# Kernel tuning notes

Measured on AMD Instinct MI355X. Metric: run time of the kernel, lower is better.

## Reference

```python
import jax, jax.numpy as jnp
import numpy as np

N = 200000
MESH = (128, 128, 128)   # mesh_dimensions
P = 4                    # spline_order
ALPHA = 0.35             # Ewald splitting parameter (1/Angstrom)
KE = 14.3996             # coulomb_constant, eV*A/e^2
BOX = 128.0              # cubic box edge, Angstrom


def _bspline(u, n):
    """Cardinal B-spline M_n(u), support [0, n]. Recursion depth = n-2 (static)."""
    if n == 2:
        return jnp.clip(1.0 - jnp.abs(u - 1.0), 0.0, 1.0)
    return (u * _bspline(u, n - 1) + (n - u) * _bspline(u - 1.0, n - 1)) / (n - 1)


def _spread_weights(frac_d, K):
    """Per-dimension P spline weights and wrapped grid indices for each atom."""
    u = frac_d * K
    base = jnp.floor(u)
    j = jnp.arange(P, dtype=frac_d.dtype)
    # evaluation points t_j = (u - base) + (P-1) - j, each in (0, P)
    t = (u - base)[:, None] + (P - 1) - j                      # [N, P]
    w = _bspline(t, P)                                         # [N, P]
    idx = (base.astype(jnp.int32)[:, None] - (P - 1)
           + jnp.arange(P, dtype=jnp.int32)) % K               # [N, P]
    return w, idx


def _bmod2(K):
    """|b(m)|^2 Euler exponential-spline factors for one mesh dimension."""
    m = (jnp.fft.fftfreq(K) * K).astype(jnp.float32)
    k = jnp.arange(P - 1, dtype=jnp.float32)
    Mv = _bspline(k + 1.0, P)                                  # M_P(1..P-1)
    D = (Mv[None, :] * jnp.exp(2j * jnp.pi * m[:, None] * k[None, :] / K)).sum(-1)
    return (1.0 / jnp.maximum(jnp.abs(D) ** 2, 1e-12)).astype(jnp.float32)


def _pme_energy(positions, charges, cell):
    Kx, Ky, Kz = MESH
    cellinv = jnp.linalg.inv(cell)
    V = jnp.abs(jnp.linalg.det(cell))
    frac = (positions @ cellinv) % 1.0                         # [N, 3]

    # --- B-spline charge spreading (scatter) ---
    wx, ix = _spread_weights(frac[:, 0], Kx)
    wy, iy = _spread_weights(frac[:, 1], Ky)
    wz, iz = _spread_weights(frac[:, 2], Kz)
    w3 = (charges[:, None, None, None]
          * wx[:, :, None, None] * wy[:, None, :, None] * wz[:, None, None, :])
    lin = (ix[:, :, None, None] * Ky + iy[:, None, :, None]) * Kz + iz[:, None, None, :]
    Q = (jnp.zeros(Kx * Ky * Kz, dtype=positions.dtype)
         .at[lin.reshape(-1)].add(w3.reshape(-1))
         .reshape(MESH))

    # --- reciprocal space ---
    S = jnp.fft.fftn(Q)
    S2 = (S * jnp.conj(S)).real                                # |F[Q]|^2
    b3 = (_bmod2(Kx)[:, None, None] * _bmod2(Ky)[None, :, None]
          * _bmod2(Kz)[None, None, :])
    mx = (jnp.fft.fftfreq(Kx) * Kx).astype(positions.dtype)
    my = (jnp.fft.fftfreq(Ky) * Ky).astype(positions.dtype)
    mz = (jnp.fft.fftfreq(Kz) * Kz).astype(positions.dtype)
    mg = jnp.stack(jnp.meshgrid(mx, my, mz, indexing='ij'), axis=-1)  # [Kx,Ky,Kz,3]
    kvec = 2.0 * jnp.pi * jnp.einsum('xyzm,nm->xyzn', mg, cellinv)
    k2 = (kvec ** 2).sum(-1)
    G = jnp.where(k2 > 0.0,
                  jnp.exp(-k2 / (4.0 * ALPHA ** 2)) / jnp.where(k2 > 0.0, k2, 1.0),
                  0.0)
    e_rec = KE * (2.0 * jnp.pi / V) * (G * b3 * S2).sum()
    e_self = -KE * ALPHA / jnp.sqrt(jnp.pi).astype(positions.dtype) * (charges ** 2).sum()
    return e_rec + e_self


def setup_inputs() -> dict:
    key = jax.random.key(0)
    k1, k2 = jax.random.split(key)
    positions = jax.random.uniform(k1, (N, 3), dtype=jnp.float32) * BOX
    charges = jax.random.normal(k2, (N,), dtype=jnp.float32) * 0.5
    charges = charges - charges.mean()   # neutral system (k=0 mode excluded)
    cell = jnp.eye(3, dtype=jnp.float32) * BOX
    return {"positions": positions, "charges": charges, "cell": cell}


def reference(positions, charges, cell):
    # energy [B=1, 1] and analytic forces [N, 3] via force gather (dE/dr)
    e, g = jax.value_and_grad(lambda p: _pme_energy(p, charges, cell))(positions)
    return (jnp.reshape(e, (1, 1)), -g)
```

## Files before the change

### kernel.cpp

```cpp
#include <hip/hip_runtime.h>

#define KDIM 128
#define NTOT (KDIM * KDIM * KDIM)
#define BPD 16
#define NBINS (BPD * BPD * BPD)
#define TILE_D 11
#define T2 (TILE_D * TILE_D)
#define TILE_N (TILE_D * TILE_D * TILE_D)
#define TPAD 1332
#define TSTRIDE 1344
#define CHUNK 256
#define NZKEEP 65
#define NSCALE_BLK (NZKEEP * 8)
#define ST 17
#define ZST 17

static constexpr float PI_F = 3.14159265358979323846f;
static constexpr float TWO_PI_F = 6.28318530717958647692f;
static constexpr float KE_F = 14.3996f;
static constexpr float ALPHA_F = 0.35f;

__device__ __forceinline__ int brev7(int i) { return (int)(__brev((unsigned)i) >> 25); }

struct pf4 { float a, b, c, d; };
__device__ __forceinline__ pf4 ld4u(const float* p) {
    pf4 v;
    __builtin_memcpy(&v, p, 16);
    return v;
}

__device__ __forceinline__ void inv3x3(const float* c, float* inv, float* adet) {
    float a00 = c[0], a01 = c[1], a02 = c[2];
    float a10 = c[3], a11 = c[4], a12 = c[5];
    float a20 = c[6], a21 = c[7], a22 = c[8];
    float det = a00 * (a11 * a22 - a12 * a21) - a01 * (a10 * a22 - a12 * a20) +
                a02 * (a10 * a21 - a11 * a20);
    float id = 1.0f / det;
    inv[0] = (a11 * a22 - a12 * a21) * id;
    inv[1] = (a02 * a21 - a01 * a22) * id;
    inv[2] = (a01 * a12 - a02 * a11) * id;
    inv[3] = (a12 * a20 - a10 * a22) * id;
    inv[4] = (a00 * a22 - a02 * a20) * id;
    inv[5] = (a02 * a10 - a00 * a12) * id;
    inv[6] = (a10 * a21 - a11 * a20) * id;
    inv[7] = (a01 * a20 - a00 * a21) * id;
    inv[8] = (a00 * a11 - a01 * a10) * id;
    *adet = fabsf(det);
}

__device__ __forceinline__ void bspline4(float f, float* w, float* dw) {
    float f2 = f * f, f3 = f2 * f;
    float omf = 1.0f - f;
    w[0] = omf * omf * omf * (1.0f / 6.0f);
    w[1] = (3.0f * f3 - 6.0f * f2 + 4.0f) * (1.0f / 6.0f);
    w[2] = (-3.0f * f3 + 3.0f * f2 + 3.0f * f + 1.0f) * (1.0f / 6.0f);
    w[3] = f3 * (1.0f / 6.0f);
    dw[0] = -0.5f * omf * omf;
    dw[1] = 1.5f * f2 - 2.0f * f;
    dw[2] = -1.5f * f2 + f + 0.5f;
    dw[3] = 0.5f * f2;
}

__device__ __forceinline__ void atom_base(const float* __restrict__ pos, const float* inv,
                                          int i, int base[3], float fpart[3]) {
    float p0 = pos[3 * i], p1 = pos[3 * i + 1], p2 = pos[3 * i + 2];
#pragma unroll
    for (int d = 0; d < 3; d++) {
        float fr = p0 * inv[d] + p1 * inv[3 + d] + p2 * inv[6 + d];
        fr -= floorf(fr);
        float u = fr * (float)KDIM;
        float bs = floorf(u);
        fpart[d] = u - bs;
        int b = (int)bs;
        base[d] = b & (KDIM - 1);
    }
}

__device__ __forceinline__ float bmod2f(int x) {
    float th = (TWO_PI_F / (float)KDIM) * (float)x;
    float s1, c1, s2, c2;
    __sincosf(th, &s1, &c1);
    __sincosf(th + th, &s2, &c2);
    float dr = 0.16666667f + 0.66666667f * c1 + 0.16666667f * c2;
    float di = 0.66666667f * s1 + 0.16666667f * s2;
    float d2 = dr * dr + di * di;
    return 1.0f / fmaxf(d2, 1e-12f);
}

__global__ __launch_bounds__(256) void zero_tbl_kernel(int* __restrict__ counts,
                                                       int* __restrict__ cursor,
                                                       float* __restrict__ mtblS,
                                                       float* __restrict__ btblS) {
    int i = blockIdx.x * 256 + threadIdx.x;
    if (i < NBINS) {
        counts[i] = 0;
        cursor[i] = 0;
    }
    if (blockIdx.x == 0 && threadIdx.x < KDIM) {
        int r = brev7(threadIdx.x);
        mtblS[threadIdx.x] = (float)(r < 64 ? r : r - 128);
        btblS[threadIdx.x] = bmod2f(r);
    }
}

__global__ __launch_bounds__(256) void hist_kernel(const float* __restrict__ pos,
                                                   const float* __restrict__ chg,
                                                   const float* __restrict__ cell,
                                                   int* __restrict__ counts,
                                                   float* __restrict__ q2_part, int n) {
    __shared__ float hred[4];
    int i = blockIdx.x * blockDim.x + threadIdx.x;
    float q2 = 0.0f;
    if (i < n) {
        float inv[9], det;
        inv3x3(cell, inv, &det);
        int base[3];
        float fp[3];
        atom_base(pos, inv, i, base, fp);
        int bid = ((base[0] >> 3) << 8) | ((base[1] >> 3) << 4) | (base[2] >> 3);
        atomicAdd(&counts[bid], 1);
        float qi = chg[i];
        q2 = qi * qi;
    }
#pragma unroll
    for (int off = 32; off; off >>= 1) q2 += __shfl_down(q2, off);
    if ((threadIdx.x & 63) == 0) hred[threadIdx.x >> 6] = q2;
    __syncthreads();
    if (threadIdx.x == 0) q2_part[blockIdx.x] = hred[0] + hred[1] + hred[2] + hred[3];
}

__global__ __launch_bounds__(256) void scan_kernel(const int* __restrict__ counts,
                                                   int* __restrict__ starts) {
    __shared__ int part[256];
    int tid = threadIdx.x;
    int local[NBINS / 256];
    int sum = 0;
#pragma unroll
    for (int k = 0; k < NBINS / 256; k++) {
        local[k] = counts[tid * (NBINS / 256) + k];
        sum += local[k];
    }
    part[tid] = sum;
    __syncthreads();
    if (tid == 0) {
        int acc = 0;
        for (int i = 0; i < 256; i++) {
            int t = part[i];
            part[i] = acc;
            acc += t;
        }
        starts[NBINS] = acc;
    }
    __syncthreads();
    int acc = part[tid];
#pragma unroll
    for (int k = 0; k < NBINS / 256; k++) {
        starts[tid * (NBINS / 256) + k] = acc;
        acc += local[k];
    }
}

__global__ __launch_bounds__(256) void scatter_kernel(const float* __restrict__ pos,
                                                      const float* __restrict__ chg,
                                                      const float* __restrict__ cell,
                                                      const int* __restrict__ starts,
                                                      int* __restrict__ cursor,
                                                      float* __restrict__ records,
                                                      int* __restrict__ binatoms, int n) {
    int i = blockIdx.x * blockDim.x + threadIdx.x;
    if (i >= n) return;
    float inv[9], det;
    inv3x3(cell, inv, &det);
    int base[3];
    float fp[3];
    atom_base(pos, inv, i, base, fp);
    int bid = ((base[0] >> 3) << 8) | ((base[1] >> 3) << 4) | (base[2] >> 3);
    int slot = atomicAdd(&cursor[bid], 1) + starts[bid];
    binatoms[slot] = i;
    int loc = (base[0] & 7) | ((base[1] & 7) << 4) | ((base[2] & 7) << 8);
    float4* rec = (float4*)(records + (size_t)slot * 8);
    rec[0] = make_float4(fp[0], fp[1], fp[2], chg[i]);
    rec[1] = make_float4(__int_as_float(loc), 0.0f, 0.0f, 0.0f);
}

__global__ __launch_bounds__(256) void spread_bins_kernel(
    const float* __restrict__ records, const int* __restrict__ starts,
    float* __restrict__ tiles) {
    __shared__ float tile4[4 * TPAD];
    __shared__ float4 arec[CHUNK * 4];
    int tid = threadIdx.x;
    int bid = blockIdx.x;
    for (int i = tid; i < 4 * TPAD; i += 256) tile4[i] = 0.0f;
    int s = starts[bid], e = starts[bid + 1];
    int w = tid >> 6, l = tid & 63;
    int j0 = l >> 4, j1 = (l >> 2) & 3, j2 = l & 3;
    int joff = j0 * T2 + j1 * TILE_D + j2;
    float* mytile = tile4 + w * TPAD;
    for (int c0 = s; c0 < e; c0 += CHUNK) {
        int cnt = min(CHUNK, e - c0);
        __syncthreads();
        if (tid < cnt) {
            const float4* rp = (const float4*)records + (size_t)(c0 + tid) * 2;
            float4 r0 = rp[0];
            float4 r1 = rp[1];
            float wv[4], dv[4];
            bspline4(r0.x, wv, dv);
            arec[tid * 4 + 0] =
                make_float4(r0.w * wv[0], r0.w * wv[1], r0.w * wv[2], r0.w * wv[3]);
            bspline4(r0.y, wv, dv);
            arec[tid * 4 + 1] = make_float4(wv[0], wv[1], wv[2], wv[3]);
            bspline4(r0.z, wv, dv);
            arec[tid * 4 + 2] = make_float4(wv[0], wv[1], wv[2], wv[3]);
            arec[tid * 4 + 3] = r1;
        }
        __syncthreads();
        for (int a = w; a < cnt; a += 4) {
            const float* A = (const float*)&arec[a << 2];
            float val = A[j0] * A[4 + j1] * A[8 + j2];
            int lc = __float_as_int(A[12]);
            int tb = (lc & 15) * T2 + ((lc >> 4) & 15) * TILE_D + ((lc >> 8) & 15);
            mytile[tb + joff] += val;
        }
    }
    __syncthreads();
    float* tout = tiles + (size_t)bid * TSTRIDE;
    for (int i = tid; i < TILE_N; i += 256)
        tout[i] = tile4[i] + tile4[TPAD + i] + tile4[2 * TPAD + i] + tile4[3 * TPAD + i];
}

__device__ __forceinline__ float2 cmul(float2 a, float cs, float sn) {
    return make_float2(a.x * cs - a.y * sn, a.x * sn + a.y * cs);
}

__device__ __forceinline__ void wave_fft128_dif(float2& v0, float2& v1, int l, float sign) {
    {
        float ang = sign * (PI_F / 64.0f) * (float)l;
        float sn, cs;
        __sincosf(ang, &sn, &cs);
        float2 d = make_float2(v0.x - v1.x, v0.y - v1.y);
        v0 = make_float2(v0.x + v1.x, v0.y + v1.y);
        v1 = cmul(d, cs, sn);
    }
#pragma unroll
    for (int m = 32; m >= 1; m >>= 1) {
        float ang = sign * (PI_F / (float)m) * (float)(l & (m - 1));
        float sn, cs;
        __sincosf(ang, &sn, &cs);
        bool hi = (l & m) != 0;
        float2 p0, p1;
        p0.x = __shfl_xor(v0.x, m);
        p0.y = __shfl_xor(v0.y, m);
        p1.x = __shfl_xor(v1.x, m);
        p1.y = __shfl_xor(v1.y, m);
        float2 a0 = hi ? cmul(make_float2(p0.x - v0.x, p0.y - v0.y), cs, sn)
                       : make_float2(v0.x + p0.x, v0.y + p0.y);
        float2 a1 = hi ? cmul(make_float2(p1.x - v1.x, p1.y - v1.y), cs, sn)
                       : make_float2(v1.x + p1.x, v1.y + p1.y);
        v0 = a0;
        v1 = a1;
    }
}

__device__ __forceinline__ void wave_fft128_dit(float2& v0, float2& v1, int l, float sign) {
#pragma unroll
    for (int m = 1; m <= 32; m <<= 1) {
        float2 p0, p1;
        p0.x = __shfl_xor(v0.x, m);
        p0.y = __shfl_xor(v0.y, m);
        p1.x = __shfl_xor(v1.x, m);
        p1.y = __shfl_xor(v1.y, m);
        float ang = sign * (PI_F / (float)m) * (float)(l & (m - 1));
        float sn, cs;
        __sincosf(ang, &sn, &cs);
        bool hi = (l & m) != 0;
        float2 o0 = hi ? v0 : p0, e0 = hi ? p0 : v0;
        float2 o1 = hi ? v1 : p1, e1 = hi ? p1 : v1;
        float2 t0 = cmul(o0, cs, sn);
        float2 t1 = cmul(o1, cs, sn);
        float s = hi ? -1.0f : 1.0f;
        v0 = make_float2(e0.x + s * t0.x, e0.y + s * t0.y);
        v1 = make_float2(e1.x + s * t1.x, e1.y + s * t1.y);
    }
    float ang = sign * (PI_F / 64.0f) * (float)l;
    float sn, cs;
    __sincosf(ang, &sn, &cs);
    float2 t = cmul(v1, cs, sn);
    float2 e = v0;
    v0 = make_float2(e.x + t.x, e.y + t.y);
    v1 = make_float2(e.x - t.x, e.y - t.y);
}

__device__ __forceinline__ float merge_val(const float* __restrict__ tiles, int nx, int ny,
                                           const int* bxs, const int* lxs, const int* bys,
                                           const int* lys, int gz) {
    int bz = gz >> 3, oz = gz & 7;
    int nz = (oz >= 5) ? 2 : 1;
    int bzs[2] = {bz, (bz + 1) & 15}, lzs[2] = {oz + 3, oz - 5};
    float v = 0.0f;
    for (int i = 0; i < nx; i++)
        for (int j = 0; j < ny; j++) {
            int bxy = (bxs[i] << 8) | (bys[j] << 4);
            int lo = lxs[i] * T2 + lys[j] * TILE_D;
            for (int k = 0; k < nz; k++)
                v += tiles[(size_t)(bxy | bzs[k]) * TSTRIDE + lo + lzs[k]];
        }
    return v;
}

__global__ __launch_bounds__(512) void fft_z_merge(const float* __restrict__ tiles,
                                                   float2* __restrict__ C_t) {
    __shared__ float tr[128 * 9], ti[128 * 9];
    int w = threadIdx.x >> 6, l = threadIdx.x & 63;
    int line = (blockIdx.x << 3) + w;
    int gx = line >> 7, gy = line & 127;
    int bx = gx >> 3, ox = gx & 7;
    int by = gy >> 3, oy = gy & 7;
    int nx = (ox >= 5) ? 2 : 1, ny = (oy >= 5) ? 2 : 1;
    int bxs[2] = {bx, (bx + 1) & 15}, lxs[2] = {ox + 3, ox - 5};
    int bys[2] = {by, (by + 1) & 15}, lys[2] = {oy + 3, oy - 5};
    float m0 = merge_val(tiles, nx, ny, bxs, lxs, bys, lys, l);
    float m1 = merge_val(tiles, nx, ny, bxs, lxs, bys, lys, l + 64);
    tr[l * 9 + w] = m0;
    ti[l * 9 + w] = 0.0f;
    tr[(l + 64) * 9 + w] = m1;
    ti[(l + 64) * 9 + w] = 0.0f;
    int r = brev7(l);
    float2 v0 = make_float2(tr[r * 9 + w], 0.0f);
    float2 v1 = make_float2(tr[(r + 1) * 9 + w], 0.0f);
    wave_fft128_dit(v0, v1, l, -1.0f);
    tr[l * 9 + w] = v0.x;
    ti[l * 9 + w] = v0.y;
    tr[(l + 64) * 9 + w] = v1.x;
    ti[(l + 64) * 9 + w] = v1.y;
    __syncthreads();
    int xy0 = blockIdx.x << 3;
#pragma unroll
    for (int k = 0; k < 2; k++) {
        int e = threadIdx.x + (k << 9);
        int ss = e >> 3, wl = e & 7;
        if (ss < NZKEEP)
            C_t[(size_t)ss * (KDIM * KDIM) + xy0 + wl] =
                make_float2(tr[ss * 9 + wl], ti[ss * 9 + wl]);
    }
}

template <int DIF>
__global__ __launch_bounds__(512) void fft_y(float2* __restrict__ C_t) {
    int w = threadIdx.x >> 6, l = threadIdx.x & 63;
    int line = (blockIdx.x << 3) + w;
    int base = line << 7;
    float2 v0, v1;
    if (DIF) {
        v0 = C_t[base + l];
        v1 = C_t[base + l + 64];
        wave_fft128_dif(v0, v1, l, -1.0f);
    } else {
        int r = brev7(l);
        float4 f = ((const float4*)C_t)[(line << 6) + (r >> 1)];
        v0 = make_float2(f.x, f.y);
        v1 = make_float2(f.z, f.w);
        wave_fft128_dit(v0, v1, l, 1.0f);
    }
    C_t[base + l] = v0;
    C_t[base + l + 64] = v1;
}

__global__ __launch_bounds__(512) void fft_x_scale(float2* __restrict__ C_t,
                                                   const float* __restrict__ cell,
                                                   const float* __restrict__ mtblS,
                                                   const float* __restrict__ btblS,
                                                   float* __restrict__ scale_part) {
    __shared__ float2 lds[128 * ST];
    __shared__ float red[8];
    int tid = threadIdx.x;
    int s = blockIdx.x >> 3;
    int y0 = (blockIdx.x & 7) << 4;
    int base = s * (KDIM * KDIM) + y0;
#pragma unroll
    for (int k = 0; k < 2; k++) {
        int e = tid + (k << 9);
        int ll = e >> 3, zq = e & 7;
        float4 f = ((const float4*)C_t)[(base >> 1) + ll * 64 + zq];
        lds[ll * ST + 2 * zq] = make_float2(f.x, f.y);
        lds[ll * ST + 2 * zq + 1] = make_float2(f.z, f.w);
    }
    __syncthreads();
    int w = tid >> 6, l = tid & 63;
    float inv[9], det;
    inv3x3(cell, inv, &det);
    float mz = (s == 64) ? -64.0f : (float)s;
    float bz = bmod2f(s);
    float wz = (s == 0 || s == 64) ? 1.0f : 2.0f;
    float contrib = 0.0f;
#pragma unroll
    for (int c = 0; c < 2; c++) {
        int zt = (w << 1) | c;
        float2 v0 = lds[l * ST + zt];
        float2 v1 = lds[(l + 64) * ST + zt];
        wave_fft128_dif(v0, v1, l, -1.0f);
        int yp = y0 + zt;
        float my = mtblS[yp];
        float byz = btblS[yp] * bz;
#pragma unroll
        for (int h = 0; h < 2; h++) {
            int xs = l + (h << 6);
            float mx = mtblS[xs];
            float kx = TWO_PI_F * (mx * inv[0] + my * inv[1] + mz * inv[2]);
            float ky = TWO_PI_F * (mx * inv[3] + my * inv[4] + mz * inv[5]);
            float kz = TWO_PI_F * (mx * inv[6] + my * inv[7] + mz * inv[8]);
            float k2 = kx * kx + ky * ky + kz * kz;
            float A = 0.0f;
            if (k2 > 0.0f)
                A = __expf(-k2 / (4.0f * ALPHA_F * ALPHA_F)) / k2 * btblS[xs] * byz;
            float2& v = h ? v1 : v0;
            contrib += A * (v.x * v.x + v.y * v.y);
            v.x *= A;
            v.y *= A;
        }
        wave_fft128_dit(v0, v1, l, 1.0f);
        lds[l * ST + zt] = v0;
        lds[(l + 64) * ST + zt] = v1;
    }
    contrib *= wz;
#pragma unroll
    for (int off = 32; off; off >>= 1) contrib += __shfl_down(contrib, off);
    if (l == 0) red[w] = contrib;
    __syncthreads();
    if (tid == 0) {
        float v = 0.0f;
        for (int i = 0; i < 8; i++) v += red[i];
        scale_part[blockIdx.x] = v;
    }
#pragma unroll
    for (int k = 0; k < 2; k++) {
        int e = tid + (k << 9);
        int ll = e >> 3, zq = e & 7;
        float2 a = lds[ll * ST + 2 * zq];
        float2 b = lds[ll * ST + 2 * zq + 1];
        ((float4*)C_t)[(base >> 1) + ll * 64 + zq] = make_float4(a.x, a.y, b.x, b.y);
    }
}

__global__ __launch_bounds__(512) void fft_z_phi(const float2* __restrict__ C_t,
                                                 float* __restrict__ phi) {
    __shared__ float tr[NZKEEP * ZST], ti[NZKEEP * ZST];
    int tid = threadIdx.x;
    int xy0 = blockIdx.x << 4;
    for (int e = tid; e < NZKEEP * 16; e += 512) {
        int ss = e >> 4, q = e & 15;
        float2 v = C_t[(size_t)ss * (KDIM * KDIM) + xy0 + q];
        tr[ss * ZST + q] = v.x;
        ti[ss * ZST + q] = v.y;
    }
    __syncthreads();
    int w = tid >> 6, l = tid & 63;
    int r = brev7(l);
#pragma unroll
    for (int c0 = 0; c0 < 2; c0++) {
        int c = (w << 1) | c0;
        float2 v0, v1;
        if (r <= 62) {
            v0 = make_float2(tr[r * ZST + c], ti[r * ZST + c]);
            v1 = make_float2(tr[(r + 1) * ZST + c], ti[(r + 1) * ZST + c]);
        } else if (r == 64) {
            v0 = make_float2(tr[64 * ZST + c], ti[64 * ZST + c]);
            v1 = make_float2(tr[63 * ZST + c], -ti[63 * ZST + c]);
        } else {
            int m0 = 128 - r;
            v0 = make_float2(tr[m0 * ZST + c], -ti[m0 * ZST + c]);
            v1 = make_float2(tr[(m0 - 1) * ZST + c], -ti[(m0 - 1) * ZST + c]);
        }
        wave_fft128_dit(v0, v1, l, 1.0f);
        phi[(xy0 + c) * KDIM + l] = v0.x;
        phi[(xy0 + c) * KDIM + l + 64] = v1.x;
    }
}

__global__ __launch_bounds__(256) void gather_kernel(
    const float* __restrict__ pos, const float* __restrict__ chg,
    const float* __restrict__ cell, const int* __restrict__ binatoms,
    const float* __restrict__ phi, const float* __restrict__ scale_part,
    const float* __restrict__ q2_part, int nq2, float* __restrict__ out, int n) {
    __shared__ double sd[256];
    if (blockIdx.x == 0) {
        int tid = threadIdx.x;
        double es = 0.0;
        for (int i = tid; i < NSCALE_BLK; i += 256) es += (double)scale_part[i];
        double q2 = 0.0;
        for (int i = tid; i < nq2; i += 256) q2 += (double)q2_part[i];
        sd[tid] = es;
        __syncthreads();
        for (int s = 128; s; s >>= 1) {
            if (tid < s) sd[tid] += sd[tid + s];
            __syncthreads();
        }
        double esum = sd[0];
        __syncthreads();
        sd[tid] = q2;
        __syncthreads();
        for (int s = 128; s; s >>= 1) {
            if (tid < s) sd[tid] += sd[tid + s];
            __syncthreads();
        }
        if (tid == 0) {
            float invf[9], det;
            inv3x3(cell, invf, &det);
            double cc = (double)KE_F * 2.0 * 3.14159265358979323846 / (double)det;
            double e = cc * esum -
                       (double)KE_F * (double)ALPHA_F / 1.7724538509055160273 * sd[0];
            out[0] = (float)e;
        }
    }
    int a = blockIdx.x * blockDim.x + threadIdx.x;
    if (a >= n) return;
    int i = binatoms[a];
    float inv[9], det;
    inv3x3(cell, inv, &det);
    int base[3];
    float fp[3];
    atom_base(pos, inv, i, base, fp);
    float wx[4], wy[4], wzv[4], dxv[4], dyv[4], dzv[4];
    bspline4(fp[0], wx, dxv);
    bspline4(fp[1], wy, dyv);
    bspline4(fp[2], wzv, dzv);
    int ix[4], iy[4];
#pragma unroll
    for (int j = 0; j < 4; j++) {
        ix[j] = (base[0] - 3 + j + KDIM) & (KDIM - 1);
        iy[j] = (base[1] - 3 + j + KDIM) & (KDIM - 1);
    }
    float acc0 = 0.0f, acc1 = 0.0f, acc2 = 0.0f;
    int bz = base[2];
    if (bz >= 3) {
        int z0 = bz - 3;
#pragma unroll
        for (int j0 = 0; j0 < 4; j0++) {
            int r0 = ix[j0] << 14;
            float wxx = wx[j0], dxx = dxv[j0];
#pragma unroll
            for (int j1 = 0; j1 < 4; j1++) {
                pf4 p = ld4u(&phi[r0 + (iy[j1] << 7) + z0]);
                float sw = p.a * wzv[0] + p.b * wzv[1] + p.c * wzv[2] + p.d * wzv[3];
                float sdz = p.a * dzv[0] + p.b * dzv[1] + p.c * dzv[2] + p.d * dzv[3];
                float wyy = wy[j1];
                acc0 += sw * dxx * wyy;
                acc1 += sw * wxx * dyv[j1];
                acc2 += sdz * wxx * wyy;
            }
        }
    } else {
        int iz[4];
#pragma unroll
        for (int j = 0; j < 4; j++) iz[j] = (bz - 3 + j + KDIM) & (KDIM - 1);
#pragma unroll
        for (int j0 = 0; j0 < 4; j0++) {
            int r0 = ix[j0] << 14;
            float wxx = wx[j0], dxx = dxv[j0];
#pragma unroll
            for (int j1 = 0; j1 < 4; j1++) {
                int r1 = r0 + (iy[j1] << 7);
                float sw = 0.0f, sdz = 0.0f;
#pragma unroll
                for (int j2 = 0; j2 < 4; j2++) {
                    float p = phi[r1 + iz[j2]];
                    sw += p * wzv[j2];
                    sdz += p * dzv[j2];
                }
                float wyy = wy[j1];
                acc0 += sw * dxx * wyy;
                acc1 += sw * wxx * dyv[j1];
                acc2 += sdz * wxx * wyy;
            }
        }
    }
    float qi = chg[i];
    float c = KE_F * TWO_PI_F / det;
    float fac = -2.0f * c * qi * (float)KDIM;
    out[1 + 3 * i + 0] = fac * (acc0 * inv[0] + acc1 * inv[1] + acc2 * inv[2]);
    out[1 + 3 * i + 1] = fac * (acc0 * inv[3] + acc1 * inv[4] + acc2 * inv[5]);
    out[1 + 3 * i + 2] = fac * (acc0 * inv[6] + acc1 * inv[7] + acc2 * inv[8]);
}

extern "C" void kernel_launch(void* const* d_in, const int* in_sizes, int n_in,
                              void* d_out, int out_size, void* d_ws, size_t ws_size,
                              hipStream_t stream) {
    const float* pos = (const float*)d_in[0];
    const float* chg = (const float*)d_in[1];
    const float* cell = (const float*)d_in[2];
    float* out = (float*)d_out;
    int n = in_sizes[1];
    int nb = (n + 255) / 256;

    char* w = (char*)d_ws;
    float2* C_t = (float2*)w;
    size_t off = (size_t)NTOT * sizeof(float2);
    float* tiles = (float*)(w + off);
    off += (size_t)NBINS * TSTRIDE * sizeof(float);
    int* counts = (int*)(w + off);
    off += NBINS * sizeof(int);
    int* cursor = (int*)(w + off);
    off += NBINS * sizeof(int);
    int* starts = (int*)(w + off);
    off += (NBINS + 1) * sizeof(int);
    int* binatoms = (int*)(w + off);
    off += (size_t)n * sizeof(int);
    float* scale_part = (float*)(w + off);
    off += NSCALE_BLK * sizeof(float);
    float* q2_part = (float*)(w + off);
    off += (size_t)nb * sizeof(float);
    float* mtblS = (float*)(w + off);
    off += KDIM * sizeof(float);
    float* btblS = (float*)(w + off);

    float* records = (float*)C_t;
    float* phi = (float*)tiles;

    zero_tbl_kernel<<<(NBINS + 255) / 256, 256, 0, stream>>>(counts, cursor, mtblS, btblS);
    hist_kernel<<<nb, 256, 0, stream>>>(pos, chg, cell, counts, q2_part, n);
    scan_kernel<<<1, 256, 0, stream>>>(counts, starts);
    scatter_kernel<<<nb, 256, 0, stream>>>(pos, chg, cell, starts, cursor, records,
                                           binatoms, n);
    spread_bins_kernel<<<NBINS, 256, 0, stream>>>(records, starts, tiles);

    fft_z_merge<<<2048, 512, 0, stream>>>(tiles, C_t);
    fft_y<1><<<NZKEEP * KDIM / 8, 512, 0, stream>>>(C_t);
    fft_x_scale<<<NSCALE_BLK, 512, 0, stream>>>(C_t, cell, mtblS, btblS, scale_part);
    fft_y<0><<<NZKEEP * KDIM / 8, 512, 0, stream>>>(C_t);
    fft_z_phi<<<KDIM * KDIM / 16, 512, 0, stream>>>(C_t, phi);

    gather_kernel<<<nb, 256, 0, stream>>>(pos, chg, cell, binatoms, phi, scale_part,
                                          q2_part, nb, out, n);
}
```

Measured before the change: 140.1 us.

## Fuse inverse y-FFT and z-FFT into one per-x-plane kernel using LDS

Replaces the separate inverse y-FFT pass and the z-FFT-to-phi pass with a single kernel in which each 1024-thread block loads a whole x-plane (65 half-spectrum z rows by 128 y) into LDS. It then runs the y FFTs and the Hermitian-extended z FFTs from that shared buffer. This removes one full global read and write of the complex spectrum plus a kernel launch. In exchange it launches only 128 blocks with about 66 KB of LDS each, which sharply reduces occupancy and parallelism on a GPU with many CUs.

```diff
diff --git a/kernel.cpp b/kernel.cpp
--- a/kernel.cpp
+++ b/kernel.cpp
@@ -13,7 +13,7 @@
 #define NZKEEP 65
 #define NSCALE_BLK (NZKEEP * 8)
 #define ST 17
-#define ZST 17
+#define YST 129
 
 static constexpr float PI_F = 3.14159265358979323846f;
 static constexpr float TWO_PI_F = 6.28318530717958647692f;
@@ -344,23 +344,13 @@
     }
 }
 
-template <int DIF>
-__global__ __launch_bounds__(512) void fft_y(float2* __restrict__ C_t) {
+__global__ __launch_bounds__(512) void fft_y_fwd(float2* __restrict__ C_t) {
     int w = threadIdx.x >> 6, l = threadIdx.x & 63;
     int line = (blockIdx.x << 3) + w;
     int base = line << 7;
-    float2 v0, v1;
-    if (DIF) {
-        v0 = C_t[base + l];
-        v1 = C_t[base + l + 64];
-        wave_fft128_dif(v0, v1, l, -1.0f);
-    } else {
-        int r = brev7(l);
-        float4 f = ((const float4*)C_t)[(line << 6) + (r >> 1)];
-        v0 = make_float2(f.x, f.y);
-        v1 = make_float2(f.z, f.w);
-        wave_fft128_dit(v0, v1, l, 1.0f);
-    }
+    float2 v0 = C_t[base + l];
+    float2 v1 = C_t[base + l + 64];
+    wave_fft128_dif(v0, v1, l, -1.0f);
     C_t[base + l] = v0;
     C_t[base + l + 64] = v1;
 }
@@ -441,38 +431,50 @@
     }
 }
 
-__global__ __launch_bounds__(512) void fft_z_phi(const float2* __restrict__ C_t,
-                                                 float* __restrict__ phi) {
-    __shared__ float tr[NZKEEP * ZST], ti[NZKEEP * ZST];
+__global__ __launch_bounds__(1024) void fft_yz_inv(const float2* __restrict__ C_t,
+                                                   float* __restrict__ phi) {
+    __shared__ float tr[NZKEEP * YST];
+    __shared__ float ti[NZKEEP * YST];
     int tid = threadIdx.x;
-    int xy0 = blockIdx.x << 4;
-    for (int e = tid; e < NZKEEP * 16; e += 512) {
-        int ss = e >> 4, q = e & 15;
-        float2 v = C_t[(size_t)ss * (KDIM * KDIM) + xy0 + q];
-        tr[ss * ZST + q] = v.x;
-        ti[ss * ZST + q] = v.y;
+    int x = blockIdx.x;
+    for (int e = tid; e < NZKEEP * KDIM; e += 1024) {
+        int ss = e >> 7, y = e & 127;
+        float2 v = C_t[(size_t)ss * (KDIM * KDIM) + (x << 7) + y];
+        tr[ss * YST + y] = v.x;
+        ti[ss * YST + y] = v.y;
     }
     __syncthreads();
     int w = tid >> 6, l = tid & 63;
     int r = brev7(l);
-#pragma unroll
-    for (int c0 = 0; c0 < 2; c0++) {
-        int c = (w << 1) | c0;
+    for (int ss = w; ss < NZKEEP; ss += 16) {
+        float* rr = tr + ss * YST;
+        float* ri = ti + ss * YST;
+        float2 v0 = make_float2(rr[r], ri[r]);
+        float2 v1 = make_float2(rr[r + 1], ri[r + 1]);
+        wave_fft128_dit(v0, v1, l, 1.0f);
+        rr[l] = v0.x;
+        ri[l] = v0.y;
+        rr[l + 64] = v1.x;
+        ri[l + 64] = v1.y;
+    }
+    __syncthreads();
+    for (int y = w; y < KDIM; y += 16) {
         float2 v0, v1;
         if (r <= 62) {
-            v0 = make_float2(tr[r * ZST + c], ti[r * ZST + c]);
-            v1 = make_float2(tr[(r + 1) * ZST + c], ti[(r + 1) * ZST + c]);
+            v0 = make_float2(tr[r * YST + y], ti[r * YST + y]);
+            v1 = make_float2(tr[(r + 1) * YST + y], ti[(r + 1) * YST + y]);
         } else if (r == 64) {
-            v0 = make_float2(tr[64 * ZST + c], ti[64 * ZST + c]);
-            v1 = make_float2(tr[63 * ZST + c], -ti[63 * ZST + c]);
+            v0 = make_float2(tr[64 * YST + y], ti[64 * YST + y]);
+            v1 = make_float2(tr[63 * YST + y], -ti[63 * YST + y]);
         } else {
             int m0 = 128 - r;
-            v0 = make_float2(tr[m0 * ZST + c], -ti[m0 * ZST + c]);
-            v1 = make_float2(tr[(m0 - 1) * ZST + c], -ti[(m0 - 1) * ZST + c]);
+            v0 = make_float2(tr[m0 * YST + y], -ti[m0 * YST + y]);
+            v1 = make_float2(tr[(m0 - 1) * YST + y], -ti[(m0 - 1) * YST + y]);
         }
         wave_fft128_dit(v0, v1, l, 1.0f);
-        phi[(xy0 + c) * KDIM + l] = v0.x;
-        phi[(xy0 + c) * KDIM + l + 64] = v1.x;
+        float* po = phi + ((size_t)(x << 7) + y) * KDIM;
+        po[l] = v0.x;
+        po[l + 64] = v1.x;
     }
 }
 
@@ -623,10 +625,9 @@
     spread_bins_kernel<<<NBINS, 256, 0, stream>>>(records, starts, tiles);
 
     fft_z_merge<<<2048, 512, 0, stream>>>(tiles, C_t);
-    fft_y<1><<<NZKEEP * KDIM / 8, 512, 0, stream>>>(C_t);
+    fft_y_fwd<<<NZKEEP * KDIM / 8, 512, 0, stream>>>(C_t);
     fft_x_scale<<<NSCALE_BLK, 512, 0, stream>>>(C_t, cell, mtblS, btblS, scale_part);
-    fft_y<0><<<NZKEEP * KDIM / 8, 512, 0, stream>>>(C_t);
-    fft_z_phi<<<KDIM * KDIM / 16, 512, 0, stream>>>(C_t, phi);
+    fft_yz_inv<<<KDIM, 1024, 0, stream>>>(C_t, phi);
 
     gather_kernel<<<nb, 256, 0, stream>>>(pos, chg, cell, binatoms, phi, scale_part,
                                           q2_part, nb, out, n);
```

After: 144.0 us. 2.8% more time.
